# Performance work log

Hardware: AMD Instinct MI355X
Metric: run time of the kernel (lower is better)

Reference implementation:

```python
import jax, jax.numpy as jnp
import numpy as np

BS = 8            # self.b from __init__
NSAMPLE = 32      # self.nsample
EPS_TCR = 0.2     # TotalCodingRate eps
COS_EPS = 1e-8    # torch cosine_similarity eps


def setup_inputs() -> dict:
    key = jax.random.key(0)
    k0, k1, k2, k3, k4 = jax.random.split(key, 5)
    B, N, C = 8, 8192, 64
    return {
        "logits": jax.random.normal(k0, (B, N, C), jnp.float32),
        "logits1": jax.random.normal(k1, (B, N, C), jnp.float32),
        "p0first": jax.random.uniform(k2, (B, N, 3), jnp.float32),
        "p0sec": jax.random.uniform(k3, (B, N, 3), jnp.float32),
        "orixyz": jax.random.uniform(k4, (B, N, 3), jnp.float32),
    }


def _fps(p, m):
    # furthest point sampling, seed = point 0; p: [b,n,3] -> idx [b,m] int32
    b, n, _ = p.shape
    batch = jnp.arange(b)
    d0 = jnp.sum((p - p[:, :1]) ** 2, -1)  # [b,n] sq dist to seed

    def step(dist, _):
        nxt = jnp.argmax(dist, axis=1)                 # [b]
        pn = p[batch, nxt]                             # [b,3]
        dist = jnp.minimum(dist, jnp.sum((p - pn[:, None]) ** 2, -1))
        return dist, nxt

    _, idxs = jax.lax.scan(step, d0, None, length=m - 1)  # [m-1,b]
    return jnp.concatenate(
        [jnp.zeros((b, 1), jnp.int32), idxs.T.astype(jnp.int32)], axis=1)


def _knn_idx(q, s, k):
    # q: [b,m,3] queries, s: [b,n,3] support -> [b,m,k] neighbor indices
    d = (jnp.sum(q * q, -1)[:, :, None] + jnp.sum(s * s, -1)[:, None, :]
         - 2.0 * jnp.einsum('bmd,bnd->bmn', q, s))
    _, idx = jax.lax.top_k(-d, k)  # smallest distances
    return idx


def _group_losses(fi, fj, c):
    # fi: [b,m,c] center feats, fj: [b,m,k,c] neighbor feats
    # per group: datatemp = cat(fj, fi) -> [K=k+1, c]
    D = jnp.concatenate([fj, fi[:, :, None, :]], axis=2)  # [b,m,K,c]
    avg = D.mean(axis=2, keepdims=True)                   # [b,m,1,c]
    num = jnp.sum(D * avg, -1)                            # [b,m,K]
    den = jnp.maximum(
        jnp.linalg.norm(D, axis=-1) * jnp.linalg.norm(avg, axis=-1), COS_EPS)
    loss_contract = -(num / den).mean(axis=2)             # [b,m] (Similarity_Loss)
    # TotalCodingRate on each single row z: -0.5*logdet(I + (c/(BS*eps)) z z^T)
    #   = -0.5*log(1 + (c/(BS*eps)) ||z||^2)   (rank-1 identity)
    scalar = c / (BS * EPS_TCR)
    loss_tcr = (-0.5 * jnp.log1p(scalar * jnp.sum(D * D, -1))).mean(axis=2)
    return jnp.sum(200.0 * loss_contract + 1.0 * loss_tcr, axis=1)  # [b]


def reference(logits, logits1, p0first, p0sec, orixyz):
    b, n, c = logits.shape
    ds = n // 16  # downsample

    # global per-point cosine loss
    num = jnp.sum(logits * logits1, -1)
    den = jnp.maximum(
        jnp.linalg.norm(logits, axis=-1) * jnp.linalg.norm(logits1, axis=-1),
        COS_EPS)
    globalpointloss = -jnp.mean(num / den)

    idx = _fps(p0first, ds)   # [b,ds]
    idx1 = _fps(p0sec, ds)
    new_p = jnp.take_along_axis(p0first, idx[..., None], axis=1)   # [b,ds,3]
    new_p1 = jnp.take_along_axis(p0sec, idx1[..., None], axis=1)
    fi = jnp.take_along_axis(logits, idx[..., None], axis=1)       # [b,ds,c]
    fi1 = jnp.take_along_axis(logits1, idx1[..., None], axis=1)

    ki = _knn_idx(new_p, p0first, NSAMPLE)    # [b,ds,k]
    ki1 = _knn_idx(new_p1, p0sec, NSAMPLE)
    fj = jax.vmap(lambda f, i: f[i])(logits, ki)    # [b,ds,k,c]
    fj1 = jax.vmap(lambda f, i: f[i])(logits1, ki1)

    # per-batch summed group-inner losses (both views)
    S = _group_losses(fi, fj, c) + _group_losses(fi1, fj1, c)  # [b]

    # faithful to original: running total divided by downsample each batch iter
    def fold(g, s):
        return (g + s) / ds, None
    groupinnerloss, _ = jax.lax.scan(fold, jnp.float32(0.0), S)
    groupinnerloss = groupinnerloss / b

    # original returns globalpointloss + groupinnerloss + groupinnerloss
    # (groupouterloss is computed but never used in the returned loss)
    return globalpointloss + groupinnerloss + groupinnerloss
```

## Files before the change

### kernel.cpp

```cpp
#include <hip/hip_runtime.h>
#include <cstdint>

#define NPTS 8192
#define NB 8
#define DS 512
#define CF 64
#define KNN 32
#define NFPS 16
#define NWORK 240
#define NCOSI 64
#define NITEMS (NCOSI + 2 * NB * DS)
#define DYNLDS 98304

typedef float v2f __attribute__((ext_vector_type(2)));
typedef unsigned long long ull;

__device__ __forceinline__ float wave_max63(float x) {
  int v;
  v = __builtin_amdgcn_update_dpp(0, __float_as_int(x), 0x111, 0xf, 0xf, true); x = fmaxf(x, __int_as_float(v));
  v = __builtin_amdgcn_update_dpp(0, __float_as_int(x), 0x112, 0xf, 0xf, true); x = fmaxf(x, __int_as_float(v));
  v = __builtin_amdgcn_update_dpp(0, __float_as_int(x), 0x114, 0xf, 0xf, true); x = fmaxf(x, __int_as_float(v));
  v = __builtin_amdgcn_update_dpp(0, __float_as_int(x), 0x118, 0xf, 0xf, true); x = fmaxf(x, __int_as_float(v));
  v = __builtin_amdgcn_update_dpp(0, __float_as_int(x), 0x142, 0xf, 0xf, true); x = fmaxf(x, __int_as_float(v));
  v = __builtin_amdgcn_update_dpp(0, __float_as_int(x), 0x143, 0xf, 0xf, true); x = fmaxf(x, __int_as_float(v));
  return x;
}

__device__ __forceinline__ unsigned wave_umin63(unsigned x) {
  unsigned v;
  v = (unsigned)__builtin_amdgcn_update_dpp(-1, (int)x, 0x111, 0xf, 0xf, false); x = (v < x) ? v : x;
  v = (unsigned)__builtin_amdgcn_update_dpp(-1, (int)x, 0x112, 0xf, 0xf, false); x = (v < x) ? v : x;
  v = (unsigned)__builtin_amdgcn_update_dpp(-1, (int)x, 0x114, 0xf, 0xf, false); x = (v < x) ? v : x;
  v = (unsigned)__builtin_amdgcn_update_dpp(-1, (int)x, 0x118, 0xf, 0xf, false); x = (v < x) ? v : x;
  v = (unsigned)__builtin_amdgcn_update_dpp(-1, (int)x, 0x142, 0xf, 0xf, false); x = (v < x) ? v : x;
  v = (unsigned)__builtin_amdgcn_update_dpp(-1, (int)x, 0x143, 0xf, 0xf, false); x = (v < x) ? v : x;
  return x;
}

__device__ __forceinline__ float wave_sum_bcast(float x) {
  int v;
  v = __builtin_amdgcn_update_dpp(0, __float_as_int(x), 0x111, 0xf, 0xf, true); x += __int_as_float(v);
  v = __builtin_amdgcn_update_dpp(0, __float_as_int(x), 0x112, 0xf, 0xf, true); x += __int_as_float(v);
  v = __builtin_amdgcn_update_dpp(0, __float_as_int(x), 0x114, 0xf, 0xf, true); x += __int_as_float(v);
  v = __builtin_amdgcn_update_dpp(0, __float_as_int(x), 0x118, 0xf, 0xf, true); x += __int_as_float(v);
  v = __builtin_amdgcn_update_dpp(0, __float_as_int(x), 0x142, 0xf, 0xf, true); x += __int_as_float(v);
  v = __builtin_amdgcn_update_dpp(0, __float_as_int(x), 0x143, 0xf, 0xf, true); x += __int_as_float(v);
  return __int_as_float(__builtin_amdgcn_readlane(__float_as_int(x), 63));
}

__global__ __launch_bounds__(64) void zero_kernel(float* __restrict__ acc) {
  if (threadIdx.x < 16) acc[threadIdx.x] = 0.0f;
}

__global__ __launch_bounds__(512, 2) void fused_kernel(
    const float* __restrict__ logits, const float* __restrict__ logits1,
    const float* __restrict__ p0first, const float* __restrict__ p0sec,
    int* __restrict__ idxbuf, float* __restrict__ acc,
    int* __restrict__ done, float* __restrict__ out) {
  extern __shared__ char smem[];
  __shared__ __align__(16) ull wslot[2][8];
  __shared__ int wtot[8];
  __shared__ int s_bl[2];
  __shared__ int ctr, eqctr, s_center;
  __shared__ float wloss[8];

  const int blk = blockIdx.x;
  const int t = threadIdx.x;

  if (blk < NFPS) {
    float* ldsP = (float*)smem;
    const int view = blk >> 3, b = blk & 7;
    const float* p = (view ? p0sec : p0first) + (size_t)b * NPTS * 3;
    int* idx_out = idxbuf + blk * DS;
    v2f px2[8], py2[8], pz2[8], dist2[8];
#pragma unroll
    for (int j = 0; j < 8; ++j) {
      int e0 = j * 512 + t, e1 = (j + 8) * 512 + t;
      px2[j] = (v2f){p[e0 * 3 + 0], p[e1 * 3 + 0]};
      py2[j] = (v2f){p[e0 * 3 + 1], p[e1 * 3 + 1]};
      pz2[j] = (v2f){p[e0 * 3 + 2], p[e1 * 3 + 2]};
      dist2[j] = (v2f){3.4e38f, 3.4e38f};
      ldsP[e0 * 3 + 0] = px2[j].x; ldsP[e1 * 3 + 0] = px2[j].y;
      ldsP[e0 * 3 + 1] = py2[j].x; ldsP[e1 * 3 + 1] = py2[j].y;
      ldsP[e0 * 3 + 2] = pz2[j].x; ldsP[e1 * 3 + 2] = pz2[j].y;
    }
#pragma unroll
    for (int j = 0; j < 8; ++j) {
      asm("" : "+v"(px2[j]), "+v"(py2[j]), "+v"(pz2[j]));
    }
    if (t == 0)
      __hip_atomic_store(&idx_out[0], 0, __ATOMIC_RELAXED, __HIP_MEMORY_SCOPE_AGENT);
    float wx = p[0], wy = p[1], wz = p[2];
    const int lane = t & 63, wave = t >> 6;
    __syncthreads();
    for (int it = 0; it < DS - 1; ++it) {
      v2f wx2 = (v2f){wx, wx}, wy2 = (v2f){wy, wy}, wz2 = (v2f){wz, wz};
      v2f lm2 = (v2f){-1.0f, -1.0f};
#pragma unroll
      for (int j = 0; j < 8; ++j) {
        v2f dx = px2[j] - wx2, dy = py2[j] - wy2, dz = pz2[j] - wz2;
        v2f nd = dx * dx + dy * dy + dz * dz;
        v2f d = __builtin_elementwise_min(dist2[j], nd);
        dist2[j] = d;
        lm2 = __builtin_elementwise_max(lm2, d);
      }
      float lm = fmaxf(lm2.x, lm2.y);
      float wmv = wave_max63(lm);
      float wm = __int_as_float(__builtin_amdgcn_readlane(__float_as_int(wmv), 63));
      int jbest = 0;
#pragma unroll
      for (int jp = 15; jp >= 0; --jp) {
        int j = jp & 7, h = jp >> 3;
        float dv = h ? dist2[j].y : dist2[j].x;
        if (dv == lm) jbest = jp;
      }
      unsigned ev = (lm == wm) ? (unsigned)(jbest * 512 + t) : 0xffffffffu;
      unsigned evm = wave_umin63(ev);
      unsigned emin = (unsigned)__builtin_amdgcn_readlane((int)evm, 63);
      if (lane == 0)
        wslot[it & 1][wave] =
            (((ull)__float_as_uint(wm)) << 32) | (ull)(8191u - emin);
      __syncthreads();
      {
        const ull* ws = wslot[it & 1];
        ull k0 = ws[0], k1 = ws[1], k2 = ws[2], k3 = ws[3];
        ull k4 = ws[4], k5 = ws[5], k6 = ws[6], k7 = ws[7];
        ull a0 = k0 > k1 ? k0 : k1, a1 = k2 > k3 ? k2 : k3;
        ull a2 = k4 > k5 ? k4 : k5, a3 = k6 > k7 ? k6 : k7;
        ull b0 = a0 > a1 ? a0 : a1, b1 = a2 > a3 ? a2 : a3;
        ull kb = b0 > b1 ? b0 : b1;
        unsigned e = 8191u - (unsigned)(kb & 0xffffffffu);
        if (t == 0)
          __hip_atomic_store(&idx_out[it + 1], (int)e, __ATOMIC_RELAXED,
                             __HIP_MEMORY_SCOPE_AGENT);
        wx = ldsP[e * 3 + 0]; wy = ldsP[e * 3 + 1]; wz = ldsP[e * 3 + 2];
      }
    }
  } else {
    int* hb0 = (int*)smem;
    int* hb1 = (int*)(smem + 16384);
    float* Drows = (float*)(smem + 32768);
    int* nbr = (int*)(smem + 41216);
    int* eq = (int*)(smem + 41344);
    const int lane = t & 63, wave = t >> 6;
    const int w0 = blk - NFPS;
    for (int item = w0; item < NITEMS; item += NWORK) {
      if (item < NCOSI) {
        float cv = 0.0f;
#pragma unroll
        for (int rr = 0; rr < 2; ++rr) {
          int row = item * 1024 + rr * 512 + t;
          const float4* A = (const float4*)(logits + (size_t)row * CF);
          const float4* Bv = (const float4*)(logits1 + (size_t)row * CF);
          float ab = 0.f, aa = 0.f, bb = 0.f;
#pragma unroll
          for (int i = 0; i < 16; ++i) {
            float4 a = A[i], c4 = Bv[i];
            ab += a.x * c4.x + a.y * c4.y + a.z * c4.z + a.w * c4.w;
            aa += a.x * a.x + a.y * a.y + a.z * a.z + a.w * a.w;
            bb += c4.x * c4.x + c4.y * c4.y + c4.z * c4.z + c4.w * c4.w;
          }
          cv += ab / fmaxf(sqrtf(aa) * sqrtf(bb), 1e-8f);
        }
        cv = wave_sum_bcast(cv);
        if (lane == 0) wloss[wave] = cv;
        __syncthreads();
        if (t == 0) {
          float s = 0.f;
#pragma unroll
          for (int w = 0; w < 8; ++w) s += wloss[w];
          atomicAdd(&acc[0], s);
        }
        __syncthreads();
      } else {
        const int qi2 = item - NCOSI;
        const int m = qi2 >> 4, pair = qi2 & 15;
        const int g = pair * DS + m;
        const int view = pair >> 3, b = pair & 7;
        const float* p = (view ? p0sec : p0first) + (size_t)b * NPTS * 3;
        float f48[48];
        {
          const float4* p4 = (const float4*)p;
#pragma unroll
          for (int i = 0; i < 12; ++i) {
            float4 v4 = p4[t * 12 + i];
            f48[i * 4 + 0] = v4.x; f48[i * 4 + 1] = v4.y;
            f48[i * 4 + 2] = v4.z; f48[i * 4 + 3] = v4.w;
          }
        }
        for (int k = t; k < 4096; k += 512) hb0[k] = 0;
        if (t == 0) {
          int ce;
          while ((unsigned)(ce = __hip_atomic_load(&idxbuf[g], __ATOMIC_RELAXED,
                                                   __HIP_MEMORY_SCOPE_AGENT)) >= 8192u)
            __builtin_amdgcn_s_sleep(2);
          s_center = ce;
        }
        __syncthreads();
        const int ci = s_center;
        const float qx = p[ci * 3], qy = p[ci * 3 + 1], qz = p[ci * 3 + 2];
        const float qq = qx * qx + qy * qy + qz * qz;
        const int cpy = (t & 1) << 11;
        unsigned sk[16];
#pragma unroll
        for (int j = 0; j < 16; ++j) {
          float sx = f48[j * 3], sy = f48[j * 3 + 1], sz = f48[j * 3 + 2];
          float ss = sx * sx + sy * sy + sz * sz;
          float dt = qx * sx + qy * sy + qz * sz;
          float d = qq + ss - 2.0f * dt;
          unsigned u = __float_as_uint(d);
          u = (u & 0x80000000u) ? ~u : (u | 0x80000000u);
          sk[j] = u;
        }
        int rrank = 31;
#pragma unroll
        for (int j = 0; j < 16; ++j) atomicAdd(&hb0[cpy + (sk[j] >> 21)], 1);
        __syncthreads();
        unsigned pA, pAB, V;
        {
          int b0 = t << 2;
          int c0 = hb0[b0] + hb0[2048 + b0];
          int c1 = hb0[b0 + 1] + hb0[2048 + b0 + 1];
          int c2 = hb0[b0 + 2] + hb0[2048 + b0 + 2];
          int c3 = hb0[b0 + 3] + hb0[2048 + b0 + 3];
          int s = c0 + c1 + c2 + c3;
          int inc = s;
#pragma unroll
          for (int o = 1; o < 64; o <<= 1) {
            int v = __shfl_up(inc, o, 64);
            if (lane >= o) inc += v;
          }
          if (lane == 63) wtot[wave] = inc;
          for (int k = t; k < 4096; k += 512) hb1[k] = 0;
          __syncthreads();
          int off = 0;
#pragma unroll
          for (int w = 0; w < 8; ++w) off += (w < wave) ? wtot[w] : 0;
          int exc = off + inc - s;
          if (rrank >= exc && rrank < exc + s) {
            int r2 = rrank - exc; int bin, less;
            if (r2 < c0) { bin = 0; less = 0; }
            else if (r2 < c0 + c1) { bin = 1; less = c0; }
            else if (r2 < c0 + c1 + c2) { bin = 2; less = c0 + c1; }
            else { bin = 3; less = c0 + c1 + c2; }
            s_bl[0] = b0 + bin; s_bl[1] = exc + less;
          }
          __syncthreads();
          pA = (unsigned)s_bl[0];
          rrank -= s_bl[1];
        }
#pragma unroll
        for (int j = 0; j < 16; ++j) {
          unsigned u = sk[j];
          if ((u >> 21) == pA) atomicAdd(&hb1[cpy + ((u >> 10) & 2047)], 1);
        }
        __syncthreads();
        {
          int b0 = t << 2;
          int c0 = hb1[b0] + hb1[2048 + b0];
          int c1 = hb1[b0 + 1] + hb1[2048 + b0 + 1];
          int c2 = hb1[b0 + 2] + hb1[2048 + b0 + 2];
          int c3 = hb1[b0 + 3] + hb1[2048 + b0 + 3];
          int s = c0 + c1 + c2 + c3;
          int inc = s;
#pragma unroll
          for (int o = 1; o < 64; o <<= 1) {
            int v = __shfl_up(inc, o, 64);
            if (lane >= o) inc += v;
          }
          if (lane == 63) wtot[wave] = inc;
          for (int k = t; k < 4096; k += 512) hb0[k] = 0;
          __syncthreads();
          int off = 0;
#pragma unroll
          for (int w = 0; w < 8; ++w) off += (w < wave) ? wtot[w] : 0;
          int exc = off + inc - s;
          if (rrank >= exc && rrank < exc + s) {
            int r2 = rrank - exc; int bin, less;
            if (r2 < c0) { bin = 0; less = 0; }
            else if (r2 < c0 + c1) { bin = 1; less = c0; }
            else if (r2 < c0 + c1 + c2) { bin = 2; less = c0 + c1; }
            else { bin = 3; less = c0 + c1 + c2; }
            s_bl[0] = b0 + bin; s_bl[1] = exc + less;
          }
          __syncthreads();
          pAB = (pA << 11) | (unsigned)s_bl[0];
          rrank -= s_bl[1];
        }
        const int cpyC = (t & 1) << 10;
#pragma unroll
        for (int j = 0; j < 16; ++j) {
          unsigned u = sk[j];
          if ((u >> 10) == pAB) atomicAdd(&hb0[cpyC + (u & 1023)], 1);
        }
        __syncthreads();
        {
          int b0 = t << 1;
          int c0 = hb0[b0] + hb0[1024 + b0];
          int c1 = hb0[b0 + 1] + hb0[1024 + b0 + 1];
          int s = c0 + c1;
          int inc = s;
#pragma unroll
          for (int o = 1; o < 64; o <<= 1) {
            int v = __shfl_up(inc, o, 64);
            if (lane >= o) inc += v;
          }
          if (lane == 63) wtot[wave] = inc;
          __syncthreads();
          int off = 0;
#pragma unroll
          for (int w = 0; w < 8; ++w) off += (w < wave) ? wtot[w] : 0;
          int exc = off + inc - s;
          if (rrank >= exc && rrank < exc + s) {
            int r2 = rrank - exc;
            if (r2 < c0) { s_bl[0] = b0; s_bl[1] = exc; }
            else { s_bl[0] = b0 + 1; s_bl[1] = exc + c0; }
          }
          if (t == 0) { ctr = 0; eqctr = 0; }
          __syncthreads();
          V = (pAB << 10) | (unsigned)s_bl[0];
          rrank -= s_bl[1];
        }
#pragma unroll
        for (int j = 0; j < 16; ++j) {
          unsigned u = sk[j];
          if (u < V) {
            int s = atomicAdd(&ctr, 1);
            nbr[s] = t * 16 + j;
          } else if (u == V) {
            int s2 = atomicAdd(&eqctr, 1);
            if (s2 < 256) eq[s2] = t * 16 + j;
          }
        }
        __syncthreads();
        if (t == 0) {
          int need = rrank + 1;
          int E = eqctr; if (E > 256) E = 256;
          int base = KNN - need;
          for (int s = 0; s < need; ++s) {
            int mi = 0;
            for (int i = 1; i < E; ++i)
              if (eq[i] < eq[mi]) mi = i;
            nbr[base + s] = eq[mi];
            eq[mi] = 0x7fffffff;
          }
        }
        __syncthreads();
        const float* f = (view ? logits1 : logits) + (size_t)b * NPTS * CF;
        for (int r = wave; r < 33; r += 8) {
          int e = (r < 32) ? nbr[r] : ci;
          Drows[r * 64 + lane] = f[(size_t)e * CF + lane];
        }
        __syncthreads();
        float avg = 0.0f;
#pragma unroll
        for (int r = 0; r < 33; ++r) avg += Drows[r * 64 + lane];
        avg *= (1.0f / 33.0f);
        float na = wave_sum_bcast(avg * avg);
        const float rsna = sqrtf(na);
        float loss = 0.0f;
        for (int r = wave; r < 33; r += 8) {
          float d = Drows[r * 64 + lane];
          float d0 = wave_sum_bcast(d * avg);
          float n0 = wave_sum_bcast(d * d);
          float den = fmaxf(sqrtf(n0) * rsna, 1e-8f);
          loss += -200.0f * (d0 / den) - 0.5f * log1pf(40.0f * n0);
        }
        if (lane == 0) wloss[wave] = loss;
        __syncthreads();
        if (t == 0) {
          float s = 0.f;
#pragma unroll
          for (int w = 0; w < 8; ++w) s += wloss[w];
          atomicAdd(&acc[1 + b], s * (1.0f / 33.0f));
        }
        __syncthreads();
      }
    }
    __syncthreads();
    if (t == 0) {
      int d = __hip_atomic_fetch_add(done, 1, __ATOMIC_ACQ_REL, __HIP_MEMORY_SCOPE_AGENT);
      if (d == NWORK - 1) {
        float a0 = __hip_atomic_load(&acc[0], __ATOMIC_ACQUIRE, __HIP_MEMORY_SCOPE_AGENT);
        float gsum = 0.0f;
        for (int bb = 0; bb < 8; ++bb) {
          float Sb = __hip_atomic_load(&acc[1 + bb], __ATOMIC_ACQUIRE, __HIP_MEMORY_SCOPE_AGENT);
          gsum = (gsum + Sb) * (1.0f / 512.0f);
        }
        gsum *= 0.125f;
        out[0] = -a0 / 65536.0f + gsum + gsum;
      }
    }
  }
}

extern "C" void kernel_launch(void* const* d_in, const int* in_sizes, int n_in,
                              void* d_out, int out_size, void* d_ws, size_t ws_size,
                              hipStream_t stream) {
  (void)in_sizes; (void)n_in; (void)out_size; (void)ws_size;
  const float* logits  = (const float*)d_in[0];
  const float* logits1 = (const float*)d_in[1];
  const float* p0first = (const float*)d_in[2];
  const float* p0sec   = (const float*)d_in[3];
  float* out = (float*)d_out;

  float* acc = (float*)d_ws;
  int* done  = (int*)d_ws + 13;
  int* idxbuf = (int*)d_ws + 16;

  zero_kernel<<<1, 64, 0, stream>>>(acc);
  fused_kernel<<<NFPS + NWORK, 512, DYNLDS, stream>>>(logits, logits1, p0first, p0sec,
                                                      idxbuf, acc, done, out);
}
```

Before: 528.0 us.

## Use contiguous per-thread point ownership and ballot-based argmax in FPS

Each thread now owns 16 contiguous points, loaded with vectorized float4 reads that also fill LDS. Because a thread's point indices now rise with its lane, the lowest-index tie-break reduces to picking the first lane via ballot/ffs, which replaces the wave-wide unsigned min DPP reduction. The per-thread max becomes a tree reduction, and only the winning lane scans its registers for the local index. This shortens the serial per-iteration critical path of the 511-step FPS loop, at the cost of a data-dependent branch in one lane.

```diff
diff --git a/kernel.cpp b/kernel.cpp
--- a/kernel.cpp
+++ b/kernel.cpp
@@ -23,17 +23,6 @@
   v = __builtin_amdgcn_update_dpp(0, __float_as_int(x), 0x118, 0xf, 0xf, true); x = fmaxf(x, __int_as_float(v));
   v = __builtin_amdgcn_update_dpp(0, __float_as_int(x), 0x142, 0xf, 0xf, true); x = fmaxf(x, __int_as_float(v));
   v = __builtin_amdgcn_update_dpp(0, __float_as_int(x), 0x143, 0xf, 0xf, true); x = fmaxf(x, __int_as_float(v));
-  return x;
-}
-
-__device__ __forceinline__ unsigned wave_umin63(unsigned x) {
-  unsigned v;
-  v = (unsigned)__builtin_amdgcn_update_dpp(-1, (int)x, 0x111, 0xf, 0xf, false); x = (v < x) ? v : x;
-  v = (unsigned)__builtin_amdgcn_update_dpp(-1, (int)x, 0x112, 0xf, 0xf, false); x = (v < x) ? v : x;
-  v = (unsigned)__builtin_amdgcn_update_dpp(-1, (int)x, 0x114, 0xf, 0xf, false); x = (v < x) ? v : x;
-  v = (unsigned)__builtin_amdgcn_update_dpp(-1, (int)x, 0x118, 0xf, 0xf, false); x = (v < x) ? v : x;
-  v = (unsigned)__builtin_amdgcn_update_dpp(-1, (int)x, 0x142, 0xf, 0xf, false); x = (v < x) ? v : x;
-  v = (unsigned)__builtin_amdgcn_update_dpp(-1, (int)x, 0x143, 0xf, 0xf, false); x = (v < x) ? v : x;
   return x;
 }
 
@@ -72,54 +61,67 @@
     const int view = blk >> 3, b = blk & 7;
     const float* p = (view ? p0sec : p0first) + (size_t)b * NPTS * 3;
     int* idx_out = idxbuf + blk * DS;
+    const int lane = t & 63, wave = t >> 6;
     v2f px2[8], py2[8], pz2[8], dist2[8];
-#pragma unroll
-    for (int j = 0; j < 8; ++j) {
-      int e0 = j * 512 + t, e1 = (j + 8) * 512 + t;
-      px2[j] = (v2f){p[e0 * 3 + 0], p[e1 * 3 + 0]};
-      py2[j] = (v2f){p[e0 * 3 + 1], p[e1 * 3 + 1]};
-      pz2[j] = (v2f){p[e0 * 3 + 2], p[e1 * 3 + 2]};
-      dist2[j] = (v2f){3.4e38f, 3.4e38f};
-      ldsP[e0 * 3 + 0] = px2[j].x; ldsP[e1 * 3 + 0] = px2[j].y;
-      ldsP[e0 * 3 + 1] = py2[j].x; ldsP[e1 * 3 + 1] = py2[j].y;
-      ldsP[e0 * 3 + 2] = pz2[j].x; ldsP[e1 * 3 + 2] = pz2[j].y;
+    {
+      float f48[48];
+      const float4* p4 = (const float4*)p;
+      float4* l4 = (float4*)ldsP;
+#pragma unroll
+      for (int i = 0; i < 12; ++i) {
+        float4 v4 = p4[t * 12 + i];
+        l4[t * 12 + i] = v4;
+        f48[i * 4 + 0] = v4.x; f48[i * 4 + 1] = v4.y;
+        f48[i * 4 + 2] = v4.z; f48[i * 4 + 3] = v4.w;
+      }
+#pragma unroll
+      for (int g = 0; g < 8; ++g) {
+        px2[g] = (v2f){f48[6 * g + 0], f48[6 * g + 3]};
+        py2[g] = (v2f){f48[6 * g + 1], f48[6 * g + 4]};
+        pz2[g] = (v2f){f48[6 * g + 2], f48[6 * g + 5]};
+        dist2[g] = (v2f){3.4e38f, 3.4e38f};
+      }
     }
 #pragma unroll
-    for (int j = 0; j < 8; ++j) {
-      asm("" : "+v"(px2[j]), "+v"(py2[j]), "+v"(pz2[j]));
+    for (int g = 0; g < 8; ++g) {
+      asm("" : "+v"(px2[g]), "+v"(py2[g]), "+v"(pz2[g]));
     }
     if (t == 0)
       __hip_atomic_store(&idx_out[0], 0, __ATOMIC_RELAXED, __HIP_MEMORY_SCOPE_AGENT);
     float wx = p[0], wy = p[1], wz = p[2];
-    const int lane = t & 63, wave = t >> 6;
     __syncthreads();
+
     for (int it = 0; it < DS - 1; ++it) {
       v2f wx2 = (v2f){wx, wx}, wy2 = (v2f){wy, wy}, wz2 = (v2f){wz, wz};
-      v2f lm2 = (v2f){-1.0f, -1.0f};
-#pragma unroll
-      for (int j = 0; j < 8; ++j) {
-        v2f dx = px2[j] - wx2, dy = py2[j] - wy2, dz = pz2[j] - wz2;
+#pragma unroll
+      for (int g = 0; g < 8; ++g) {
+        v2f dx = px2[g] - wx2, dy = py2[g] - wy2, dz = pz2[g] - wz2;
         v2f nd = dx * dx + dy * dy + dz * dz;
-        v2f d = __builtin_elementwise_min(dist2[j], nd);
-        dist2[j] = d;
-        lm2 = __builtin_elementwise_max(lm2, d);
-      }
-      float lm = fmaxf(lm2.x, lm2.y);
+        dist2[g] = __builtin_elementwise_min(dist2[g], nd);
+      }
+      v2f m0 = __builtin_elementwise_max(dist2[0], dist2[1]);
+      v2f m1 = __builtin_elementwise_max(dist2[2], dist2[3]);
+      v2f m2 = __builtin_elementwise_max(dist2[4], dist2[5]);
+      v2f m3 = __builtin_elementwise_max(dist2[6], dist2[7]);
+      v2f n0 = __builtin_elementwise_max(m0, m1);
+      v2f n1 = __builtin_elementwise_max(m2, m3);
+      v2f q = __builtin_elementwise_max(n0, n1);
+      float lm = fmaxf(q.x, q.y);
       float wmv = wave_max63(lm);
       float wm = __int_as_float(__builtin_amdgcn_readlane(__float_as_int(wmv), 63));
-      int jbest = 0;
-#pragma unroll
-      for (int jp = 15; jp >= 0; --jp) {
-        int j = jp & 7, h = jp >> 3;
-        float dv = h ? dist2[j].y : dist2[j].x;
-        if (dv == lm) jbest = jp;
-      }
-      unsigned ev = (lm == wm) ? (unsigned)(jbest * 512 + t) : 0xffffffffu;
-      unsigned evm = wave_umin63(ev);
-      unsigned emin = (unsigned)__builtin_amdgcn_readlane((int)evm, 63);
-      if (lane == 0)
+      ull cmask = __ballot(lm == wm);
+      int winlane = (int)__ffsll(cmask) - 1;
+      if (lane == winlane) {
+        int jbest = 0;
+#pragma unroll
+        for (int jp = 15; jp >= 0; --jp) {
+          float dv = (jp & 1) ? dist2[jp >> 1].y : dist2[jp >> 1].x;
+          if (dv == lm) jbest = jp;
+        }
+        unsigned e_best = ((unsigned)t << 4) | (unsigned)jbest;
         wslot[it & 1][wave] =
-            (((ull)__float_as_uint(wm)) << 32) | (ull)(8191u - emin);
+            (((ull)__float_as_uint(wm)) << 32) | (ull)(8191u - e_best);
+      }
       __syncthreads();
       {
         const ull* ws = wslot[it & 1];
```

Measured after the change: 524.2 us. No clear change (-0.7%).
